# Kernel optimization log

Measured on AMD Instinct MI355X. Metric: run time of the kernel, lower is better.

Reference implementation:

```python
import jax, jax.numpy as jnp
import numpy as np

B, N, DIM, H = 32, 480, 1024, 16


def setup_inputs() -> dict:
    key = jax.random.key(0)
    ks = jax.random.split(key, 7)
    s = 0.02
    return {
        "q": jax.random.normal(ks[0], (B, N, DIM), jnp.float32),
        "Wq": jax.random.normal(ks[1], (DIM, DIM), jnp.float32) * s,
        "Wk": jax.random.normal(ks[2], (DIM, DIM), jnp.float32) * s,
        "Wv": jax.random.normal(ks[3], (DIM, DIM), jnp.float32) * s,
        "pe": jax.random.normal(ks[4], (480, 480), jnp.float32),
        "Wo": jax.random.normal(ks[5], (DIM, DIM), jnp.float32) * s,
        "bo": jnp.zeros((DIM,), jnp.float32),
    }


def reference(q, Wq, Wk, Wv, pe, Wo, bo):
    b, n, dim = q.shape
    h = H
    d = dim // h
    scale = d ** -0.5
    # self-attention: k = v = q (pre-projection)
    qp = (q @ Wq.T).reshape(b, n, h, d).transpose(0, 2, 1, 3)  # b h n d
    kp = (q @ Wk.T).reshape(b, n, h, d).transpose(0, 2, 1, 3)
    vp = (q @ Wv.T).reshape(b, n, h, d).transpose(0, 2, 1, 3)
    dots = jnp.einsum("bhid,bhjd->bhij", qp, kp) * scale
    dots = dots + pe[:n, :n]  # learned additive positional bias
    attn = jax.nn.softmax(dots, axis=-1)
    out = jnp.einsum("bhij,bhjd->bhid", attn, vp)
    out = out.transpose(0, 2, 1, 3).reshape(b, n, dim)
    return out @ Wo.T + bo
```

## Files before the change

kernel.cpp:

```cpp
#include <hip/hip_runtime.h>
#include <hip/hip_bf16.h>
#include <stdint.h>

#define B_   32
#define N_   480
#define DIM_ 1024
#define H_   16
#define D_   64
#define M_   (B_*N_)
#define BH_  (B_*H_)

typedef __bf16 bf16;
typedef __bf16 bf16x4 __attribute__((ext_vector_type(4)));
typedef __bf16 bf16x8 __attribute__((ext_vector_type(8)));
typedef short  short4v __attribute__((ext_vector_type(4)));
typedef float  f32x4  __attribute__((ext_vector_type(4)));

__device__ __forceinline__ void gld_lds16(const void* g, void* l) {
    using GP = const __attribute__((address_space(1))) unsigned int*;
    using LP = __attribute__((address_space(3))) unsigned int*;
    __builtin_amdgcn_global_load_lds((GP)(uintptr_t)g, (LP)(unsigned int)(uintptr_t)l, 16, 0, 0);
}

__global__ void cvt4(const float* __restrict__ in, bf16* __restrict__ out, int n4) {
    int i = blockIdx.x * 256 + threadIdx.x;
    if (i >= n4) return;
    float4 v = ((const float4*)in)[i];
    bf16x4 o = { (bf16)v.x, (bf16)v.y, (bf16)v.z, (bf16)v.w };
    ((bf16x4*)out)[i] = o;
}

__global__ void cvtW(const float* __restrict__ Wq, const float* __restrict__ Wk,
                     const float* __restrict__ Wv, const float* __restrict__ Wo,
                     bf16* __restrict__ Wcat, bf16* __restrict__ Wob) {
    int i = blockIdx.x * 256 + threadIdx.x;
    const float* src; bf16* dst;
    switch (blockIdx.y) {
        case 0: src = Wq; dst = Wcat;                break;
        case 1: src = Wk; dst = Wcat + DIM_*DIM_;    break;
        case 2: src = Wv; dst = Wcat + 2*DIM_*DIM_;  break;
        default: src = Wo; dst = Wob;                break;
    }
    float4 v = ((const float4*)src)[i];
    bf16x4 o = { (bf16)v.x, (bf16)v.y, (bf16)v.z, (bf16)v.w };
    ((bf16x4*)dst)[i] = o;
}

__global__ __launch_bounds__(256) void gemm_qkv(const bf16* __restrict__ A, const bf16* __restrict__ Bw,
                                                bf16* __restrict__ Qp, bf16* __restrict__ Kp,
                                                bf16* __restrict__ Vt) {
    __shared__ bf16 As[128*32];
    __shared__ bf16 Bs[128*32];
    const int tid  = threadIdx.x;
    const int lane = tid & 63;
    const int wid  = tid >> 6;
    const int wm   = wid & 1, wn = wid >> 1;
    const int m0   = blockIdx.y * 128;
    const int n0   = blockIdx.x * 128;
    const int lm   = lane & 15, lq = lane >> 4;

    const int srow = wid*16 + (lane >> 2);
    const int scol = (lane & 3) * 8;
    const int aOff0 = (m0 + srow) * 1024 + scol;
    const int aOff1 = (m0 + 64 + srow) * 1024 + scol;
    const int bOff0 = (n0 + srow) * 1024 + scol;
    const int bOff1 = (n0 + 64 + srow) * 1024 + scol;
    bf16* AsW0 = &As[(wid*16)*32];
    bf16* AsW1 = &As[(64 + wid*16)*32];
    bf16* BsW0 = &Bs[(wid*16)*32];
    bf16* BsW1 = &Bs[(64 + wid*16)*32];

    f32x4 acc[4][4] = {};
    for (int k0 = 0; k0 < 1024; k0 += 32) {
        gld_lds16(A  + aOff0 + k0, AsW0);
        gld_lds16(A  + aOff1 + k0, AsW1);
        gld_lds16(Bw + bOff0 + k0, BsW0);
        gld_lds16(Bw + bOff1 + k0, BsW1);
        __syncthreads();
        bf16x8 af[4], bfr[4];
#pragma unroll
        for (int m = 0; m < 4; ++m) af[m]  = *(const bf16x8*)&As[(wm*64 + m*16 + lm)*32 + lq*8];
#pragma unroll
        for (int n = 0; n < 4; ++n) bfr[n] = *(const bf16x8*)&Bs[(wn*64 + n*16 + lm)*32 + lq*8];
#pragma unroll
        for (int m = 0; m < 4; ++m)
#pragma unroll
            for (int n = 0; n < 4; ++n)
                acc[m][n] = __builtin_amdgcn_mfma_f32_16x16x32_bf16(af[m], bfr[n], acc[m][n], 0, 0, 0);
        __syncthreads();
    }

    const int part = n0 >> 10;
    int hh[4], dd[4];
#pragma unroll
    for (int n = 0; n < 4; ++n) {
        int gn = n0 + wn*64 + n*16 + lm;
        int rem = gn & 1023;
        hh[n] = rem >> 6; dd[n] = rem & 63;
    }
#pragma unroll
    for (int m = 0; m < 4; ++m) {
#pragma unroll
        for (int r = 0; r < 4; ++r) {
            int gm = m0 + wm*64 + m*16 + lq*4 + r;
            int b  = gm / 480;
            int nn = gm - b*480;
#pragma unroll
            for (int n = 0; n < 4; ++n) {
                bf16 v = (bf16)acc[m][n][r];
                int bh = b*16 + hh[n];
                if (part == 0)      Qp[(bh*480 + nn)*64 + dd[n]] = v;
                else if (part == 1) Kp[(bh*480 + nn)*64 + dd[n]] = v;
                else                Vt[(bh*64 + dd[n])*480 + nn] = v;
            }
        }
    }
}

#define KT 96
#define KS_LD 72
#define VS_LD 104
__global__ __launch_bounds__(192) void attn(const bf16* __restrict__ Qp, const bf16* __restrict__ Kp,
                                            const bf16* __restrict__ Vt, const float* __restrict__ pe,
                                            bf16* __restrict__ O) {
    __shared__ bf16 Ks[KT*KS_LD];
    __shared__ bf16 Vs[64*VS_LD];
    const int tid  = threadIdx.x;
    const int lane = tid & 63, wid = tid >> 6;
    const int bh   = blockIdx.y;
    const int b    = bh >> 4, h = bh & 15;
    const int q0   = blockIdx.x * 48;
    const int lm   = lane & 15, lq = lane >> 4;
    const int qbase = bh * (N_ * 64);

    bf16x8 qb[2];
#pragma unroll
    for (int ks = 0; ks < 2; ++ks)
        qb[ks] = *(const bf16x8*)&Qp[qbase + (q0 + wid*16 + lm)*64 + ks*32 + lq*8];
    const float* peRow = pe + (q0 + wid*16 + lm)*480;

    f32x4 ot[4] = {};
    float lsum = 0.f;

    for (int kt = 0; kt < 5; ++kt) {
        __syncthreads();
#pragma unroll
        for (int p = 0; p < 4; ++p) {
            int c = p*192 + tid;
            int row = c >> 3, of = (c & 7) * 8;
            *(uint4*)&Ks[row*KS_LD + of] = *(const uint4*)&Kp[qbase + (kt*KT + row)*64 + of];
        }
#pragma unroll
        for (int p = 0; p < 4; ++p) {
            int c = p*192 + tid;
            int row = c / 12, of = (c % 12) * 8;
            *(uint4*)&Vs[row*VS_LD + of] = *(const uint4*)&Vt[qbase + row*480 + kt*KT + of];
        }
        __syncthreads();

        short4v pb[6];
#pragma unroll
        for (int mf = 0; mf < 6; ++mf) {
            f32x4 s = {};
#pragma unroll
            for (int ks = 0; ks < 2; ++ks) {
                bf16x8 ka = *(const bf16x8*)&Ks[(mf*16 + lm)*KS_LD + ks*32 + lq*8];
                s = __builtin_amdgcn_mfma_f32_16x16x32_bf16(ka, qb[ks], s, 0, 0, 0);
            }
            bf16x4 pv;
#pragma unroll
            for (int r = 0; r < 4; ++r) {
                float e = __expf(s[r] * 0.125f + peRow[kt*KT + mf*16 + lq*4 + r]);
                lsum += e;
                pv[r] = (bf16)e;
            }
            pb[mf] = __builtin_bit_cast(short4v, pv);
        }

#pragma unroll
        for (int df = 0; df < 4; ++df)
#pragma unroll
            for (int mf = 0; mf < 6; ++mf) {
                short4v va = *(const short4v*)&Vs[(df*16 + lm)*VS_LD + mf*16 + lq*4];
                ot[df] = __builtin_amdgcn_mfma_f32_16x16x16bf16_1k(va, pb[mf], ot[df], 0, 0, 0);
            }
    }

    lsum += __shfl_xor(lsum, 16);
    lsum += __shfl_xor(lsum, 32);
    float rl = 1.f / lsum;

    __syncthreads();
    bf16* Os = Ks;
#pragma unroll
    for (int df = 0; df < 4; ++df)
#pragma unroll
        for (int r = 0; r < 4; ++r)
            Os[(wid*16 + lm)*KS_LD + df*16 + lq*4 + r] = (bf16)(ot[df][r] * rl);
    __syncthreads();
    {
        int ql = tid >> 2, d0 = (tid & 3) * 16;
        uint4 u0 = *(const uint4*)&Os[ql*KS_LD + d0];
        uint4 u1 = *(const uint4*)&Os[ql*KS_LD + d0 + 8];
        bf16* orow = &O[(b*480 + q0 + ql)*1024 + h*64 + d0];
        *(uint4*)&orow[0] = u0;
        *(uint4*)&orow[8] = u1;
    }
}

__global__ __launch_bounds__(256) void gemm_out(const bf16* __restrict__ A, const bf16* __restrict__ Bw,
                                                const float* __restrict__ bo, float* __restrict__ out) {
    __shared__ bf16 As[128*32];
    __shared__ bf16 Bs[128*32];
    const int tid  = threadIdx.x;
    const int lane = tid & 63;
    const int wid  = tid >> 6;
    const int wm   = wid & 1, wn = wid >> 1;
    const int m0   = blockIdx.y * 128;
    const int n0   = blockIdx.x * 128;
    const int lm   = lane & 15, lq = lane >> 4;

    const int srow = wid*16 + (lane >> 2);
    const int scol = (lane & 3) * 8;
    const int aOff0 = (m0 + srow) * 1024 + scol;
    const int aOff1 = (m0 + 64 + srow) * 1024 + scol;
    const int bOff0 = (n0 + srow) * 1024 + scol;
    const int bOff1 = (n0 + 64 + srow) * 1024 + scol;
    bf16* AsW0 = &As[(wid*16)*32];
    bf16* AsW1 = &As[(64 + wid*16)*32];
    bf16* BsW0 = &Bs[(wid*16)*32];
    bf16* BsW1 = &Bs[(64 + wid*16)*32];

    f32x4 acc[4][4] = {};
    for (int k0 = 0; k0 < 1024; k0 += 32) {
        gld_lds16(A  + aOff0 + k0, AsW0);
        gld_lds16(A  + aOff1 + k0, AsW1);
        gld_lds16(Bw + bOff0 + k0, BsW0);
        gld_lds16(Bw + bOff1 + k0, BsW1);
        __syncthreads();
        bf16x8 af[4], bfr[4];
#pragma unroll
        for (int m = 0; m < 4; ++m) af[m]  = *(const bf16x8*)&As[(wm*64 + m*16 + lm)*32 + lq*8];
#pragma unroll
        for (int n = 0; n < 4; ++n) bfr[n] = *(const bf16x8*)&Bs[(wn*64 + n*16 + lm)*32 + lq*8];
#pragma unroll
        for (int m = 0; m < 4; ++m)
#pragma unroll
            for (int n = 0; n < 4; ++n)
                acc[m][n] = __builtin_amdgcn_mfma_f32_16x16x32_bf16(af[m], bfr[n], acc[m][n], 0, 0, 0);
        __syncthreads();
    }
#pragma unroll
    for (int m = 0; m < 4; ++m)
#pragma unroll
        for (int n = 0; n < 4; ++n)
#pragma unroll
            for (int r = 0; r < 4; ++r) {
                int gm = m0 + wm*64 + m*16 + lq*4 + r;
                int gn = n0 + wn*64 + n*16 + lm;
                out[gm*1024 + gn] = acc[m][n][r] + bo[gn];
            }
}

extern "C" void kernel_launch(void* const* d_in, const int* in_sizes, int n_in,
                              void* d_out, int out_size, void* d_ws, size_t ws_size,
                              hipStream_t stream) {
    const float* q  = (const float*)d_in[0];
    const float* Wq = (const float*)d_in[1];
    const float* Wk = (const float*)d_in[2];
    const float* Wv = (const float*)d_in[3];
    const float* pe = (const float*)d_in[4];
    const float* Wo = (const float*)d_in[5];
    const float* bo = (const float*)d_in[6];
    float* out = (float*)d_out;

    char* ws = (char*)d_ws;
    bf16* Abf  = (bf16*)(ws);
    bf16* Wcat = (bf16*)(ws + 31457280);
    bf16* Wob  = (bf16*)(ws + 31457280 + 6291456);
    bf16* Qp   = (bf16*)(ws + 39845888);
    bf16* Kp   = (bf16*)(ws + 71303168);
    bf16* Vt   = (bf16*)(ws + 102760448);

    cvt4<<<(M_*DIM_/4 + 255)/256, 256, 0, stream>>>(q, Abf, M_*DIM_/4);
    cvtW<<<dim3(DIM_*DIM_/4/256, 4), 256, 0, stream>>>(Wq, Wk, Wv, Wo, Wcat, Wob);

    gemm_qkv<<<dim3(24, 120), 256, 0, stream>>>(Abf, Wcat, Qp, Kp, Vt);
    attn<<<dim3(10, 512), 192, 0, stream>>>(Qp, Kp, Vt, pe, Abf);
    gemm_out<<<dim3(8, 120), 256, 0, stream>>>(Abf, Wob, bo, out);
}
```

Before: 472.7 us.

## Deepen GEMM K-tile with XOR-swizzled LDS, transpose V epilogue, widen attention blocks

Both GEMMs now stage 64-wide K tiles per barrier pair using an XOR swizzle on the LDS layout, which halves the number of syncs and is meant to reduce LDS bank conflicts. The V projection swaps the MFMA operand order so each lane writes contiguous sequence positions into the transposed Vt layout, which should make those stores coalesced. The attention kernel grows from 3 to 5 waves per block (80 queries), so each K/V tile loaded into LDS is shared by more waves. The costs are more LDS per GEMM block, which can lower occupancy, and fewer attention blocks in the grid.

```diff
diff --git a/kernel.cpp b/kernel.cpp
--- a/kernel.cpp
+++ b/kernel.cpp
@@ -46,73 +46,93 @@
     ((bf16x4*)dst)[i] = o;
 }
 
+#define GEMM_PRE()                                                            \
+    const int tid  = threadIdx.x;                                             \
+    const int lane = tid & 63;                                                \
+    const int wid  = tid >> 6;                                                \
+    const int wm   = wid & 1, wn = wid >> 1;                                  \
+    const int m0   = blockIdx.y * 128;                                        \
+    const int n0   = blockIdx.x * 128;                                        \
+    const int lm   = lane & 15, lq = lane >> 4;                               \
+    const int aLane = (lane >> 3) * 1024 + (((lane & 7) ^ (lane >> 3)) & 7) * 8; \
+    const bf16* Asrc = A  + (m0 + wid*32) * 1024 + aLane;                     \
+    const bf16* Bsrc = Bw + (n0 + wid*32) * 1024 + aLane;                     \
+    bf16* AsDst = As + (wid*32)*64;                                           \
+    bf16* BsDst = Bs + (wid*32)*64;                                           \
+    int rowA[4], rowB[4];                                                     \
+    _Pragma("unroll") for (int m = 0; m < 4; ++m) rowA[m] = (wm*64 + m*16 + lm)*64; \
+    _Pragma("unroll") for (int n = 0; n < 4; ++n) rowB[n] = (wn*64 + n*16 + lm)*64; \
+    const int sw = lm & 7;                                                    \
+    int phys[2];                                                              \
+    phys[0] = ((lq)     ^ sw) * 8;                                            \
+    phys[1] = ((4 + lq) ^ sw) * 8;
+
+#define GEMM_KLOOP(FIRST, SECOND)                                             \
+    for (int k0 = 0; k0 < 1024; k0 += 64) {                                   \
+        _Pragma("unroll") for (int j = 0; j < 4; ++j) {                       \
+            gld_lds16(Asrc + k0 + j*8192, AsDst + j*512);                     \
+            gld_lds16(Bsrc + k0 + j*8192, BsDst + j*512);                     \
+        }                                                                     \
+        __syncthreads();                                                      \
+        _Pragma("unroll") for (int ks = 0; ks < 2; ++ks) {                    \
+            bf16x8 af[4], bfr[4];                                             \
+            _Pragma("unroll") for (int m = 0; m < 4; ++m)                     \
+                af[m]  = *(const bf16x8*)&As[rowA[m] + phys[ks]];             \
+            _Pragma("unroll") for (int n = 0; n < 4; ++n)                     \
+                bfr[n] = *(const bf16x8*)&Bs[rowB[n] + phys[ks]];             \
+            _Pragma("unroll") for (int m = 0; m < 4; ++m)                     \
+                _Pragma("unroll") for (int n = 0; n < 4; ++n)                 \
+                    acc[m][n] = __builtin_amdgcn_mfma_f32_16x16x32_bf16(      \
+                        FIRST, SECOND, acc[m][n], 0, 0, 0);                   \
+        }                                                                     \
+        __syncthreads();                                                      \
+    }
+
 __global__ __launch_bounds__(256) void gemm_qkv(const bf16* __restrict__ A, const bf16* __restrict__ Bw,
                                                 bf16* __restrict__ Qp, bf16* __restrict__ Kp,
                                                 bf16* __restrict__ Vt) {
-    __shared__ bf16 As[128*32];
-    __shared__ bf16 Bs[128*32];
-    const int tid  = threadIdx.x;
-    const int lane = tid & 63;
-    const int wid  = tid >> 6;
-    const int wm   = wid & 1, wn = wid >> 1;
-    const int m0   = blockIdx.y * 128;
-    const int n0   = blockIdx.x * 128;
-    const int lm   = lane & 15, lq = lane >> 4;
-
-    const int srow = wid*16 + (lane >> 2);
-    const int scol = (lane & 3) * 8;
-    const int aOff0 = (m0 + srow) * 1024 + scol;
-    const int aOff1 = (m0 + 64 + srow) * 1024 + scol;
-    const int bOff0 = (n0 + srow) * 1024 + scol;
-    const int bOff1 = (n0 + 64 + srow) * 1024 + scol;
-    bf16* AsW0 = &As[(wid*16)*32];
-    bf16* AsW1 = &As[(64 + wid*16)*32];
-    bf16* BsW0 = &Bs[(wid*16)*32];
-    bf16* BsW1 = &Bs[(64 + wid*16)*32];
-
+    __shared__ bf16 As[128*64];
+    __shared__ bf16 Bs[128*64];
+    GEMM_PRE();
+    const int part = n0 >> 10;
     f32x4 acc[4][4] = {};
-    for (int k0 = 0; k0 < 1024; k0 += 32) {
-        gld_lds16(A  + aOff0 + k0, AsW0);
-        gld_lds16(A  + aOff1 + k0, AsW1);
-        gld_lds16(Bw + bOff0 + k0, BsW0);
-        gld_lds16(Bw + bOff1 + k0, BsW1);
-        __syncthreads();
-        bf16x8 af[4], bfr[4];
-#pragma unroll
-        for (int m = 0; m < 4; ++m) af[m]  = *(const bf16x8*)&As[(wm*64 + m*16 + lm)*32 + lq*8];
-#pragma unroll
-        for (int n = 0; n < 4; ++n) bfr[n] = *(const bf16x8*)&Bs[(wn*64 + n*16 + lm)*32 + lq*8];
-#pragma unroll
-        for (int m = 0; m < 4; ++m)
+
+    if (part != 2) {
+        GEMM_KLOOP(af[m], bfr[n]);
+        bf16* dst = (part == 0) ? Qp : Kp;
+        int hh[4], dd[4];
+#pragma unroll
+        for (int n = 0; n < 4; ++n) {
+            int rem = (n0 + wn*64 + n*16 + lm) & 1023;
+            hh[n] = rem >> 6; dd[n] = rem & 63;
+        }
+#pragma unroll
+        for (int m = 0; m < 4; ++m) {
+#pragma unroll
+            for (int r = 0; r < 4; ++r) {
+                int gm = m0 + wm*64 + m*16 + lq*4 + r;
+                int b  = gm / 480;
+                int nn = gm - b*480;
+#pragma unroll
+                for (int n = 0; n < 4; ++n)
+                    dst[((b*16 + hh[n])*480 + nn)*64 + dd[n]] = (bf16)acc[m][n][r];
+            }
+        }
+    } else {
+        GEMM_KLOOP(bfr[n], af[m]);
+#pragma unroll
+        for (int m = 0; m < 4; ++m) {
+            int gmBase = m0 + wm*64 + m*16;
+            int b  = gmBase / 480;
+            int nn = gmBase - b*480 + lm;
 #pragma unroll
             for (int n = 0; n < 4; ++n)
-                acc[m][n] = __builtin_amdgcn_mfma_f32_16x16x32_bf16(af[m], bfr[n], acc[m][n], 0, 0, 0);
-        __syncthreads();
-    }
-
-    const int part = n0 >> 10;
-    int hh[4], dd[4];
-#pragma unroll
-    for (int n = 0; n < 4; ++n) {
-        int gn = n0 + wn*64 + n*16 + lm;
-        int rem = gn & 1023;
-        hh[n] = rem >> 6; dd[n] = rem & 63;
-    }
-#pragma unroll
-    for (int m = 0; m < 4; ++m) {
-#pragma unroll
-        for (int r = 0; r < 4; ++r) {
-            int gm = m0 + wm*64 + m*16 + lq*4 + r;
-            int b  = gm / 480;
-            int nn = gm - b*480;
-#pragma unroll
-            for (int n = 0; n < 4; ++n) {
-                bf16 v = (bf16)acc[m][n][r];
-                int bh = b*16 + hh[n];
-                if (part == 0)      Qp[(bh*480 + nn)*64 + dd[n]] = v;
-                else if (part == 1) Kp[(bh*480 + nn)*64 + dd[n]] = v;
-                else                Vt[(bh*64 + dd[n])*480 + nn] = v;
-            }
+#pragma unroll
+                for (int r = 0; r < 4; ++r) {
+                    int rem = (n0 + wn*64 + n*16 + lq*4 + r) & 1023;
+                    int h = rem >> 6, d = rem & 63;
+                    Vt[((b*16 + h)*64 + d)*480 + nn] = (bf16)acc[m][n][r];
+                }
         }
     }
 }
@@ -120,7 +140,7 @@
 #define KT 96
 #define KS_LD 72
 #define VS_LD 104
-__global__ __launch_bounds__(192) void attn(const bf16* __restrict__ Qp, const bf16* __restrict__ Kp,
+__global__ __launch_bounds__(320) void attn(const bf16* __restrict__ Qp, const bf16* __restrict__ Kp,
                                             const bf16* __restrict__ Vt, const float* __restrict__ pe,
                                             bf16* __restrict__ O) {
     __shared__ bf16 Ks[KT*KS_LD];
@@ -129,30 +149,26 @@
     const int lane = tid & 63, wid = tid >> 6;
     const int bh   = blockIdx.y;
     const int b    = bh >> 4, h = bh & 15;
-    const int q0   = blockIdx.x * 48;
+    const int qblk = blockIdx.x * 80;
     const int lm   = lane & 15, lq = lane >> 4;
     const int qbase = bh * (N_ * 64);
 
     bf16x8 qb[2];
 #pragma unroll
     for (int ks = 0; ks < 2; ++ks)
-        qb[ks] = *(const bf16x8*)&Qp[qbase + (q0 + wid*16 + lm)*64 + ks*32 + lq*8];
-    const float* peRow = pe + (q0 + wid*16 + lm)*480;
+        qb[ks] = *(const bf16x8*)&Qp[qbase + (qblk + wid*16 + lm)*64 + ks*32 + lq*8];
+    const float* peRow = pe + (qblk + wid*16 + lm)*480;
 
     f32x4 ot[4] = {};
     float lsum = 0.f;
 
     for (int kt = 0; kt < 5; ++kt) {
         __syncthreads();
-#pragma unroll
-        for (int p = 0; p < 4; ++p) {
-            int c = p*192 + tid;
+        for (int c = tid; c < 768; c += 320) {
             int row = c >> 3, of = (c & 7) * 8;
             *(uint4*)&Ks[row*KS_LD + of] = *(const uint4*)&Kp[qbase + (kt*KT + row)*64 + of];
         }
-#pragma unroll
-        for (int p = 0; p < 4; ++p) {
-            int c = p*192 + tid;
+        for (int c = tid; c < 768; c += 320) {
             int row = c / 12, of = (c % 12) * 8;
             *(uint4*)&Vs[row*VS_LD + of] = *(const uint4*)&Vt[qbase + row*480 + kt*KT + of];
         }
@@ -198,58 +214,20 @@
         for (int r = 0; r < 4; ++r)
             Os[(wid*16 + lm)*KS_LD + df*16 + lq*4 + r] = (bf16)(ot[df][r] * rl);
     __syncthreads();
-    {
-        int ql = tid >> 2, d0 = (tid & 3) * 16;
-        uint4 u0 = *(const uint4*)&Os[ql*KS_LD + d0];
-        uint4 u1 = *(const uint4*)&Os[ql*KS_LD + d0 + 8];
-        bf16* orow = &O[(b*480 + q0 + ql)*1024 + h*64 + d0];
-        *(uint4*)&orow[0] = u0;
-        *(uint4*)&orow[8] = u1;
+    for (int c = tid; c < 640; c += 320) {
+        int row = c >> 3, d0 = (c & 7) * 8;
+        uint4 u = *(const uint4*)&Os[row*KS_LD + d0];
+        *(uint4*)&O[(b*480 + qblk + row)*1024 + h*64 + d0] = u;
     }
 }
 
 __global__ __launch_bounds__(256) void gemm_out(const bf16* __restrict__ A, const bf16* __restrict__ Bw,
                                                 const float* __restrict__ bo, float* __restrict__ out) {
-    __shared__ bf16 As[128*32];
-    __shared__ bf16 Bs[128*32];
-    const int tid  = threadIdx.x;
-    const int lane = tid & 63;
-    const int wid  = tid >> 6;
-    const int wm   = wid & 1, wn = wid >> 1;
-    const int m0   = blockIdx.y * 128;
-    const int n0   = blockIdx.x * 128;
-    const int lm   = lane & 15, lq = lane >> 4;
-
-    const int srow = wid*16 + (lane >> 2);
-    const int scol = (lane & 3) * 8;
-    const int aOff0 = (m0 + srow) * 1024 + scol;
-    const int aOff1 = (m0 + 64 + srow) * 1024 + scol;
-    const int bOff0 = (n0 + srow) * 1024 + scol;
-    const int bOff1 = (n0 + 64 + srow) * 1024 + scol;
-    bf16* AsW0 = &As[(wid*16)*32];
-    bf16* AsW1 = &As[(64 + wid*16)*32];
-    bf16* BsW0 = &Bs[(wid*16)*32];
-    bf16* BsW1 = &Bs[(64 + wid*16)*32];
-
+    __shared__ bf16 As[128*64];
+    __shared__ bf16 Bs[128*64];
+    GEMM_PRE();
     f32x4 acc[4][4] = {};
-    for (int k0 = 0; k0 < 1024; k0 += 32) {
-        gld_lds16(A  + aOff0 + k0, AsW0);
-        gld_lds16(A  + aOff1 + k0, AsW1);
-        gld_lds16(Bw + bOff0 + k0, BsW0);
-        gld_lds16(Bw + bOff1 + k0, BsW1);
-        __syncthreads();
-        bf16x8 af[4], bfr[4];
-#pragma unroll
-        for (int m = 0; m < 4; ++m) af[m]  = *(const bf16x8*)&As[(wm*64 + m*16 + lm)*32 + lq*8];
-#pragma unroll
-        for (int n = 0; n < 4; ++n) bfr[n] = *(const bf16x8*)&Bs[(wn*64 + n*16 + lm)*32 + lq*8];
-#pragma unroll
-        for (int m = 0; m < 4; ++m)
-#pragma unroll
-            for (int n = 0; n < 4; ++n)
-                acc[m][n] = __builtin_amdgcn_mfma_f32_16x16x32_bf16(af[m], bfr[n], acc[m][n], 0, 0, 0);
-        __syncthreads();
-    }
+    GEMM_KLOOP(af[m], bfr[n]);
 #pragma unroll
     for (int m = 0; m < 4; ++m)
 #pragma unroll
@@ -286,6 +264,6 @@
     cvtW<<<dim3(DIM_*DIM_/4/256, 4), 256, 0, stream>>>(Wq, Wk, Wv, Wo, Wcat, Wob);
 
     gemm_qkv<<<dim3(24, 120), 256, 0, stream>>>(Abf, Wcat, Qp, Kp, Vt);
-    attn<<<dim3(10, 512), 192, 0, stream>>>(Qp, Kp, Vt, pe, Abf);
+    attn<<<dim3(6, 512), 320, 0, stream>>>(Qp, Kp, Vt, pe, Abf);
     gemm_out<<<dim3(8, 120), 256, 0, stream>>>(Abf, Wob, bo, out);
 }
```

Result: faster. 414.1 us (-12.4%).
